# Performance work log

Measured on AMD Instinct MI355X. Metric: run time of the kernel, lower is better.

The kernel has to match this reference:

```python
import jax, jax.numpy as jnp
import numpy as np

B, L, PD, DIM, H, DH, DEPTH, MLP, NIMG, NCLS, TH = 2, 2048, 768, 512, 8, 64, 2, 2048, 4, 1000, 32


def _ln(x, g):
    # bias-free LayerNorm (beta buffer is zeros), eps matches torch F.layer_norm
    mu = jnp.mean(x, axis=-1, keepdims=True)
    var = jnp.var(x, axis=-1, keepdims=True)
    return (x - mu) / jnp.sqrt(var + 1e-5) * g


def _rms(x, g):
    # F.normalize(dim=-1) * sqrt(dim_head) * gamma; x: [b,h,n,dh], g: [h,1,dh]
    n = jnp.linalg.norm(x, axis=-1, keepdims=True)
    return x / jnp.maximum(n, 1e-12) * (DH ** 0.5) * g


def _attn(x, context, mask, ln_g, qg, kg, Wq, Wkv, Wo):
    b, n = x.shape[0], x.shape[1]
    xn = _ln(x, ln_g)
    kv = xn if context is None else context  # context is NOT pre-normed (matches source)
    m = kv.shape[1]
    q = (xn @ Wq).reshape(b, n, H, DH).transpose(0, 2, 1, 3)   # [b,h,n,dh]
    k, v = jnp.split(kv @ Wkv, 2, axis=-1)
    k = k.reshape(b, m, H, DH).transpose(0, 2, 1, 3)
    v = v.reshape(b, m, H, DH).transpose(0, 2, 1, 3)
    q = _rms(q, qg)
    k = _rms(k, kg)
    dots = jnp.einsum('bhid,bhjd->bhij', q, k)  # no 1/sqrt(d): QK-RMSNorm carries the scale
    neg = -jnp.finfo(dots.dtype).max
    dots = jnp.where(mask, dots, neg)
    a = jax.nn.softmax(dots, axis=-1)
    out = jnp.einsum('bhij,bhjd->bhid', a, v)
    out = out.transpose(0, 2, 1, 3).reshape(b, n, H * DH)
    return out @ Wo


def _forward(patches, ln_pe1_g, W_pe, b_pe, ln_pe2_g, pos_h_emb, pos_w_emb,
             attn_ln_g, q_g, k_g, Wq, Wkv, Wo, ff_ln_g, W1, b1, W2, b2,
             final_ln_g, pool_q, pool_ln_g, pool_q_g, pool_k_g,
             pool_Wq, pool_Wkv, pool_Wo, head_ln_g, W_head,
             pos_h, pos_w, image_ids):
    # patch embedding: LN -> Linear -> LN, then factorized 2D pos embed
    x = _ln(patches, ln_pe1_g) @ W_pe + b_pe
    x = _ln(x, ln_pe2_g)
    x = x + pos_h_emb[pos_h] + pos_w_emb[pos_w]
    # block-diagonal attention mask: tokens attend only within their image
    mask = (image_ids[:, None, :, None] == image_ids[:, None, None, :])  # [B,1,L,L]
    for i in range(DEPTH):
        x = _attn(x, None, mask, attn_ln_g[i], q_g[i], k_g[i], Wq[i], Wkv[i], Wo[i]) + x
        h = _ln(x, ff_ln_g[i]) @ W1[i] + b1[i]
        h = jax.nn.gelu(h, approximate=False)
        x = h @ W2[i] + b2[i] + x
    x = _ln(x, final_ln_g)
    # attention pooling: one learned query per packed image
    queries = jnp.broadcast_to(pool_q, (B, NIMG, DIM))
    pmask = (jnp.arange(NIMG)[None, None, :, None] == image_ids[:, None, None, :])  # [B,1,NIMG,L]
    pooled = _attn(queries, x, pmask, pool_ln_g, pool_q_g, pool_k_g, pool_Wq, pool_Wkv, pool_Wo) + queries
    return _ln(pooled, head_ln_g) @ W_head  # [B, NIMG, NCLS]


def setup_inputs() -> dict:
    key = jax.random.key(0)
    ks = jax.random.split(key, 16)
    s = 0.02
    inp = {}
    inp['patches'] = jax.random.normal(ks[0], (B, L, PD), jnp.float32)
    inp['pos_h'] = jax.random.randint(ks[1], (B, L), 0, TH)
    inp['pos_w'] = jax.random.randint(ks[2], (B, L), 0, TH)
    inp['image_ids'] = jnp.sort(jax.random.randint(ks[3], (B, L), 0, NIMG), axis=-1)
    inp['ln_pe1_g'] = jnp.ones((PD,), jnp.float32)
    inp['W_pe'] = jax.random.normal(ks[4], (PD, DIM), jnp.float32) * s
    inp['b_pe'] = jnp.zeros((DIM,), jnp.float32)
    inp['ln_pe2_g'] = jnp.ones((DIM,), jnp.float32)
    inp['pos_h_emb'] = jax.random.normal(ks[5], (TH, DIM), jnp.float32)
    inp['pos_w_emb'] = jax.random.normal(ks[6], (TH, DIM), jnp.float32)
    inp['attn_ln_g'] = jnp.ones((DEPTH, DIM), jnp.float32)
    inp['q_g'] = jnp.ones((DEPTH, H, 1, DH), jnp.float32)
    inp['k_g'] = jnp.ones((DEPTH, H, 1, DH), jnp.float32)
    inp['Wq'] = jax.random.normal(ks[7], (DEPTH, DIM, H * DH), jnp.float32) * s
    inp['Wkv'] = jax.random.normal(ks[8], (DEPTH, DIM, 2 * H * DH), jnp.float32) * s
    inp['Wo'] = jax.random.normal(ks[9], (DEPTH, H * DH, DIM), jnp.float32) * s
    inp['ff_ln_g'] = jnp.ones((DEPTH, DIM), jnp.float32)
    inp['W1'] = jax.random.normal(ks[10], (DEPTH, DIM, MLP), jnp.float32) * s
    inp['b1'] = jnp.zeros((DEPTH, MLP), jnp.float32)
    inp['W2'] = jax.random.normal(ks[11], (DEPTH, MLP, DIM), jnp.float32) * s
    inp['b2'] = jnp.zeros((DEPTH, DIM), jnp.float32)
    inp['final_ln_g'] = jnp.ones((DIM,), jnp.float32)
    inp['pool_q'] = jax.random.normal(ks[12], (DIM,), jnp.float32)
    inp['pool_ln_g'] = jnp.ones((DIM,), jnp.float32)
    inp['pool_q_g'] = jnp.ones((H, 1, DH), jnp.float32)
    inp['pool_k_g'] = jnp.ones((H, 1, DH), jnp.float32)
    inp['pool_Wq'] = jax.random.normal(ks[13], (DIM, H * DH), jnp.float32) * s
    inp['pool_Wkv'] = jax.random.normal(ks[14], (DIM, 2 * H * DH), jnp.float32) * s
    inp['pool_Wo'] = jax.random.normal(ks[15], (H * DH, DIM), jnp.float32) * s
    inp['head_ln_g'] = jnp.ones((DIM,), jnp.float32)
    inp['W_head'] = jax.random.normal(jax.random.fold_in(key, 99), (DIM, NCLS), jnp.float32) * s
    return inp


def reference(patches, pos_h, pos_w, image_ids, ln_pe1_g, W_pe, b_pe, ln_pe2_g,
              pos_h_emb, pos_w_emb, attn_ln_g, q_g, k_g, Wq, Wkv, Wo, ff_ln_g,
              W1, b1, W2, b2, final_ln_g, pool_q, pool_ln_g, pool_q_g, pool_k_g,
              pool_Wq, pool_Wkv, pool_Wo, head_ln_g, W_head):
    return _forward(patches, ln_pe1_g, W_pe, b_pe, ln_pe2_g, pos_h_emb, pos_w_emb,
                    attn_ln_g, q_g, k_g, Wq, Wkv, Wo, ff_ln_g, W1, b1, W2, b2,
                    final_ln_g, pool_q, pool_ln_g, pool_q_g, pool_k_g,
                    pool_Wq, pool_Wkv, pool_Wo, head_ln_g, W_head,
                    pos_h, pos_w, image_ids)
```

## Files before the change

kernel.cpp:

```cpp
#include <hip/hip_runtime.h>
#include <hip/hip_bf16.h>
#include <cfloat>
#include <math.h>

#define BB 2
#define LL 2048
#define PD 768
#define DIM 512
#define HH 8
#define DH 64
#define DEPTH 2
#define MLP 2048
#define NIMG 4
#define NCLS 1000
#define ROWS (BB*LL)
#define QKV (3*DIM)
#define NEGBIG (-1e30f)

typedef __hip_bfloat16 bf16;
typedef __bf16 v8bf __attribute__((ext_vector_type(8)));
typedef float f32x4 __attribute__((ext_vector_type(4)));

__device__ __forceinline__ float ldin(const void* p, size_t i, int bf) {
    return bf ? __bfloat162float(((const bf16*)p)[i]) : ((const float*)p)[i];
}
__device__ __forceinline__ float lda(const float* p, size_t i) { return p[i]; }
__device__ __forceinline__ float lda(const bf16* p, size_t i) { return __bfloat162float(p[i]); }
__device__ __forceinline__ void st(float* p, size_t i, float v) { p[i] = v; }
__device__ __forceinline__ void st(bf16* p, size_t i, float v) { p[i] = __float2bfloat16(v); }
__device__ __forceinline__ unsigned short f2bf(float x) {
    return __builtin_bit_cast(unsigned short, __float2bfloat16(x));
}
__device__ __forceinline__ float us2f(unsigned short u) {
    return __bfloat162float(__builtin_bit_cast(bf16, u));
}

__device__ __forceinline__ void stage16(const void* gsrc, void* ldst)
{
    __builtin_amdgcn_global_load_lds(
        (const __attribute__((address_space(1))) unsigned int*)(unsigned long long)gsrc,
        (__attribute__((address_space(3))) unsigned int*)(unsigned int)(unsigned long long)ldst,
        16, 0, 0);
}

__global__ void detect_dtype_kernel(const void* ones, int* flag)
{
    if (threadIdx.x == 0 && blockIdx.x == 0)
        *flag = (((const unsigned*)ones)[0] == 0x3F803F80u) ? 1 : 0;
}

__global__ void wconv_kernel(const void* __restrict__ W, int K, int N, size_t inStride,
                             bf16* __restrict__ out, size_t outOff, size_t outStride,
                             const int* dtf)
{
    __shared__ float t[32][33];
    const int bf = *dtf;
    const size_t zin = (size_t)blockIdx.z * inStride;
    const size_t zout = outOff + (size_t)blockIdx.z * outStride;
    const int kb = blockIdx.y * 32, nb = blockIdx.x * 32;
    const int tx = threadIdx.x, ty = threadIdx.y;
    #pragma unroll
    for (int u = 0; u < 4; ++u)
        t[ty + 8 * u][tx] = ldin(W, zin + (size_t)(kb + ty + 8 * u) * N + nb + tx, bf);
    __syncthreads();
    #pragma unroll
    for (int u = 0; u < 4; ++u)
        out[zout + (size_t)(nb + ty + 8 * u) * K + kb + tx] = __float2bfloat16(t[tx][ty + 8 * u]);
}

template<int RAWIN, typename TOUT>
__global__ void ln_kernel(const void* __restrict__ in, const void* __restrict__ g, size_t goff,
                          TOUT* __restrict__ out, int D, const int* dtf)
{
    __shared__ float red[16];
    const int bf = *dtf;
    const int row = blockIdx.x, tid = threadIdx.x;
    const size_t base = (size_t)row * D;
    float s = 0.f, ss = 0.f;
    for (int d = tid; d < D; d += blockDim.x) {
        float v = RAWIN ? ldin(in, base + d, bf) : ((const float*)in)[base + d];
        s += v; ss += v * v;
    }
    for (int o = 32; o; o >>= 1) { s += __shfl_xor(s, o); ss += __shfl_xor(ss, o); }
    const int wid = tid >> 6, lane = tid & 63, nw = blockDim.x >> 6;
    if (lane == 0) { red[wid] = s; red[8 + wid] = ss; }
    __syncthreads();
    if (tid == 0) {
        float a = 0.f, b = 0.f;
        for (int w = 0; w < nw; ++w) { a += red[w]; b += red[8 + w]; }
        red[0] = a; red[8] = b;
    }
    __syncthreads();
    const float mean = red[0] / D;
    const float var  = red[8] / D - mean * mean;
    const float rstd = rsqrtf(var + 1e-5f);
    for (int d = tid; d < D; d += blockDim.x) {
        float v = RAWIN ? ldin(in, base + d, bf) : ((const float*)in)[base + d];
        st(out, base + d, (v - mean) * rstd * ldin(g, goff + d, bf));
    }
}

__global__ void patch_fuse_kernel(const float* __restrict__ part,
                                  const void* __restrict__ b_pe,
                                  const void* __restrict__ g1,
                                  const void* __restrict__ phe, const void* __restrict__ pwe,
                                  const int* __restrict__ ph, const int* __restrict__ pw,
                                  const void* __restrict__ g2,
                                  float* __restrict__ x, bf16* __restrict__ xb,
                                  const int* dtf)
{
    __shared__ float red[16];
    const int bf = *dtf;
    const int row = blockIdx.x, tid = threadIdx.x;
    const size_t base = (size_t)row * DIM;
    const int wid = tid >> 6, lane = tid & 63;
    float v[2];
    float s = 0.f, ss = 0.f;
    #pragma unroll
    for (int u = 0; u < 2; ++u) {
        const int d = tid + 256 * u;
        float a = part[base + d] + part[(size_t)ROWS * DIM + base + d] + ldin(b_pe, d, bf);
        v[u] = a; s += a; ss += a * a;
    }
    for (int o = 32; o; o >>= 1) { s += __shfl_xor(s, o); ss += __shfl_xor(ss, o); }
    if (lane == 0) { red[wid] = s; red[8 + wid] = ss; }
    __syncthreads();
    if (tid == 0) {
        float a = 0.f, b = 0.f;
        for (int w2 = 0; w2 < 4; ++w2) { a += red[w2]; b += red[8 + w2]; }
        red[0] = a; red[8] = b;
    }
    __syncthreads();
    {
        const float mean = red[0] / DIM;
        const float var  = red[8] / DIM - mean * mean;
        const float rstd = rsqrtf(var + 1e-5f);
        const size_t hoff = (size_t)ph[row] * DIM, woff = (size_t)pw[row] * DIM;
        s = 0.f; ss = 0.f;
        #pragma unroll
        for (int u = 0; u < 2; ++u) {
            const int d = tid + 256 * u;
            float a = (v[u] - mean) * rstd * ldin(g1, d, bf)
                    + ldin(phe, hoff + d, bf) + ldin(pwe, woff + d, bf);
            x[base + d] = a;
            v[u] = a; s += a; ss += a * a;
        }
    }
    for (int o = 32; o; o >>= 1) { s += __shfl_xor(s, o); ss += __shfl_xor(ss, o); }
    __syncthreads();
    if (lane == 0) { red[wid] = s; red[8 + wid] = ss; }
    __syncthreads();
    if (tid == 0) {
        float a = 0.f, b = 0.f;
        for (int w2 = 0; w2 < 4; ++w2) { a += red[w2]; b += red[8 + w2]; }
        red[0] = a; red[8] = b;
    }
    __syncthreads();
    const float mean = red[0] / DIM;
    const float var  = red[8] / DIM - mean * mean;
    const float rstd = rsqrtf(var + 1e-5f);
    #pragma unroll
    for (int u = 0; u < 2; ++u) {
        const int d = tid + 256 * u;
        xb[base + d] = __float2bfloat16((v[u] - mean) * rstd * ldin(g2, d, bf));
    }
}

#define GM 128
#define GN 64
#define GK 64

template<typename TO, int EPI>
__global__ void mgemm_kernel(const bf16* __restrict__ A, const bf16* __restrict__ Wt,
                             const void* __restrict__ bias, size_t boff,
                             const float* __restrict__ resid, TO* __restrict__ out,
                             int M, int N, int K, int kc, int gelu, const int* dtf)
{
    __shared__ __align__(16) unsigned short As[2][GM][GK];
    __shared__ __align__(16) unsigned short Bs[2][GN][GK];
    const int tid = threadIdx.x;
    const int w = tid >> 6, l = tid & 63, g = l >> 4, c = l & 15;
    const int wm = (w >> 1) * 64, wn = (w & 1) * 32;
    const int m0 = blockIdx.y * GM, n0 = blockIdx.x * GN;
    const int kbeg = blockIdx.z * kc;
    const int lrow = l >> 3, lcol = (l & 7) * 8;

#define STAGE_MG(BUF, K0)                                                          \
    {                                                                              \
        _Pragma("unroll")                                                          \
        for (int u = 0; u < 4; ++u) {                                              \
            const int rr = 32 * w + 8 * u;                                         \
            stage16(A + (size_t)(m0 + rr + lrow) * K + (K0) + lcol, &As[BUF][rr][0]); \
        }                                                                          \
        _Pragma("unroll")                                                          \
        for (int u = 0; u < 2; ++u) {                                              \
            const int rr = 16 * w + 8 * u;                                         \
            stage16(Wt + (size_t)(n0 + rr + lrow) * K + (K0) + lcol, &Bs[BUF][rr][0]); \
        }                                                                          \
    }

    f32x4 acc[4][2] = {};
    const int nt = kc / GK;
    STAGE_MG(0, kbeg);
    int cur = 0;
    for (int t = 0; t < nt; ++t) {
        if (t + 1 < nt) {
            STAGE_MG(cur ^ 1, kbeg + (t + 1) * GK);
            asm volatile("s_waitcnt vmcnt(6)" ::: "memory");
        } else {
            asm volatile("s_waitcnt vmcnt(0)" ::: "memory");
        }
        __builtin_amdgcn_s_barrier();
        __builtin_amdgcn_sched_barrier(0);
        #pragma unroll
        for (int kk = 0; kk < GK; kk += 32) {
            v8bf av[4], bv[2];
            #pragma unroll
            for (int i = 0; i < 4; ++i) av[i] = *(const v8bf*)&As[cur][wm + i * 16 + c][kk + 8 * g];
            #pragma unroll
            for (int j = 0; j < 2; ++j) bv[j] = *(const v8bf*)&Bs[cur][wn + j * 16 + c][kk + 8 * g];
            #pragma unroll
            for (int i = 0; i < 4; ++i)
                #pragma unroll
                for (int j = 0; j < 2; ++j)
                    acc[i][j] = __builtin_amdgcn_mfma_f32_16x16x32_bf16(av[i], bv[j], acc[i][j], 0, 0, 0);
        }
        __builtin_amdgcn_s_barrier();
        cur ^= 1;
    }
#undef STAGE_MG

    if (EPI == 0) {
        float* po = (float*)out + (size_t)blockIdx.z * M * N;
        #pragma unroll
        for (int i = 0; i < 4; ++i) {
            const int rb = m0 + wm + i * 16 + 4 * g;
            #pragma unroll
            for (int j = 0; j < 2; ++j) {
                const int col = n0 + wn + j * 16 + c;
                #pragma unroll
                for (int r = 0; r < 4; ++r)
                    po[(size_t)(rb + r) * N + col] = acc[i][j][r];
            }
        }
    } else {
        const int bf = *dtf;
        #pragma unroll
        for (int i = 0; i < 4; ++i) {
            const int rb = m0 + wm + i * 16 + 4 * g;
            #pragma unroll
            for (int j = 0; j < 2; ++j) {
                const int col = n0 + wn + j * 16 + c;
                const float bvl = bias ? ldin(bias, boff + col, bf) : 0.f;
                #pragma unroll
                for (int r = 0; r < 4; ++r) {
                    float v = acc[i][j][r] + bvl;
                    if (gelu) v = 0.5f * v * (1.f + erff(v * 0.70710678118654752f));
                    if (resid) v += resid[(size_t)(rb + r) * N + col];
                    st(out, (size_t)(rb + r) * N + col, v);
                }
            }
        }
    }
}

__global__ void comb_ln_kernel(const float* __restrict__ part, int S,
                               const void* __restrict__ bias, size_t boff,
                               float* __restrict__ x, const void* __restrict__ g, size_t goff,
                               bf16* __restrict__ xb, const int* dtf)
{
    __shared__ float red[16];
    const int bf = *dtf;
    const int row = blockIdx.x, tid = threadIdx.x;
    const size_t base = (size_t)row * DIM;
    float v[2];
    float s = 0.f, ss = 0.f;
    #pragma unroll
    for (int u = 0; u < 2; ++u) {
        const int d = tid + 256 * u;
        float a = 0.f;
        for (int sc = 0; sc < S; ++sc) a += part[(size_t)sc * ROWS * DIM + base + d];
        if (bias) a += ldin(bias, boff + d, bf);
        a += x[base + d];
        x[base + d] = a;
        v[u] = a; s += a; ss += a * a;
    }
    for (int o = 32; o; o >>= 1) { s += __shfl_xor(s, o); ss += __shfl_xor(ss, o); }
    const int wid = tid >> 6, lane = tid & 63;
    if (lane == 0) { red[wid] = s; red[8 + wid] = ss; }
    __syncthreads();
    if (tid == 0) {
        float a = 0.f, b = 0.f;
        for (int w2 = 0; w2 < 4; ++w2) { a += red[w2]; b += red[8 + w2]; }
        red[0] = a; red[8] = b;
    }
    __syncthreads();
    const float mean = red[0] / DIM;
    const float var  = red[8] / DIM - mean * mean;
    const float rstd = rsqrtf(var + 1e-5f);
    #pragma unroll
    for (int u = 0; u < 2; ++u) {
        const int d = tid + 256 * u;
        xb[base + d] = __float2bfloat16((v[u] - mean) * rstd * ldin(g, goff + d, bf));
    }
}

#define TS 16
template<typename TA, typename TO>
__global__ void gemm_kernel(const TA* __restrict__ A, const void* __restrict__ W, size_t woff,
                            const void* __restrict__ bias, size_t boff,
                            const float* __restrict__ resid, TO* __restrict__ out,
                            int M, int N, int K, int gelu, const int* dtf)
{
    __shared__ float As[TS][TS + 1];
    __shared__ float Bs[TS][TS + 1];
    const int bf = *dtf;
    const int tx = threadIdx.x, ty = threadIdx.y;
    const int col = blockIdx.x * TS + tx;
    const int row = blockIdx.y * TS + ty;
    float acc = 0.f;
    for (int k0 = 0; k0 < K; k0 += TS) {
        const int ka = k0 + tx;
        As[ty][tx] = (row < M && ka < K) ? lda(A, (size_t)row * K + ka) : 0.f;
        const int kb = k0 + ty;
        Bs[ty][tx] = (col < N && kb < K) ? ldin(W, woff + (size_t)kb * N + col, bf) : 0.f;
        __syncthreads();
        #pragma unroll
        for (int kk = 0; kk < TS; ++kk) acc = fmaf(As[ty][kk], Bs[kk][tx], acc);
        __syncthreads();
    }
    if (row < M && col < N) {
        if (bias) acc += ldin(bias, boff + col, bf);
        if (gelu) acc = 0.5f * acc * (1.f + erff(acc * 0.70710678118654752f));
        if (resid) acc += resid[(size_t)row * N + col];
        st(out, (size_t)row * N + col, acc);
    }
}

__global__ void rms_kernel(float* __restrict__ buf, const void* __restrict__ g, size_t goff,
                           int stride, int colbase, const int* dtf)
{
    const int bf = *dtf;
    const int r = blockIdx.x, h = blockIdx.y, lane = threadIdx.x;
    float* p = buf + (size_t)r * stride + colbase + h * DH;
    const float v = p[lane];
    float ss = v * v;
    for (int o = 32; o; o >>= 1) ss += __shfl_xor(ss, o);
    const float norm = sqrtf(ss);
    const float sc = 8.0f / fmaxf(norm, 1e-12f);
    p[lane] = v * sc * ldin(g, goff + h * DH + lane, bf);
}

__global__ void rms2_kernel(bf16* __restrict__ buf, int stride,
                            const void* __restrict__ g0, size_t g0off,
                            int base1, const void* __restrict__ g1, size_t g1off,
                            int nslot, const int* dtf)
{
    const int bf = *dtf;
    const int tid = threadIdx.x;
    const int s = tid >> 4, li = tid & 15;
    if (s >= nslot) return;
    const int h = s & 7;
    const int colbase = (s < 8) ? 0 : base1;
    const void* g = (s < 8) ? g0 : g1;
    const size_t go = ((s < 8) ? g0off : g1off) + h * DH + li * 4;
    bf16* p = buf + (size_t)blockIdx.x * stride + colbase + h * DH + li * 4;
    ushort4 v = *(const ushort4*)p;
    const float f0 = us2f(v.x), f1 = us2f(v.y), f2 = us2f(v.z), f3 = us2f(v.w);
    float ss = f0 * f0 + f1 * f1 + f2 * f2 + f3 * f3;
    ss += __shfl_xor(ss, 8); ss += __shfl_xor(ss, 4);
    ss += __shfl_xor(ss, 2); ss += __shfl_xor(ss, 1);
    const float sc = 8.0f / fmaxf(sqrtf(ss), 1e-12f);
    ushort4 o;
    o.x = f2bf(f0 * sc * ldin(g, go + 0, bf));
    o.y = f2bf(f1 * sc * ldin(g, go + 1, bf));
    o.z = f2bf(f2 * sc * ldin(g, go + 2, bf));
    o.w = f2bf(f3 * sc * ldin(g, go + 3, bf));
    *(ushort4*)p = o;
}

#define QT 64
#define KT 64
#define LP 72

__global__ void flash_attn_kernel(const bf16* __restrict__ q, int qstr,
                                  const bf16* __restrict__ kpt, const bf16* __restrict__ vpt,
                                  int kvstr, const int* __restrict__ ids,
                                  const void* __restrict__ qg, const void* __restrict__ kg,
                                  size_t goff, bf16* __restrict__ out, const int* dtf)
{
    __shared__ __align__(16) unsigned short Qs[QT][LP];
    __shared__ __align__(16) unsigned short Ks[KT][LP];
    __shared__ __align__(16) unsigned short Vt[DH][LP];
    __shared__ __align__(16) unsigned short Ps[QT][LP];
    __shared__ __align__(16) int ids_s[KT];
    __shared__ __align__(16) int qids_s[QT];
    __shared__ int range_s[2];

    const int bf = *dtf;
    const int tid = threadIdx.x;
    const int bid = blockIdx.x;
    const int s0 = (bid & 7) * 64 + (bid >> 3);
    const int qb = (s0 & 31) * QT;
    const int h = (s0 >> 5) & 7;
    const int b = s0 >> 8;
    const int w = tid >> 6, l = tid & 63, g = l >> 4, c = l & 15;

    const int r4 = tid >> 2, c16 = (tid & 3) << 4;

    float gk[16];
    #pragma unroll
    for (int j = 0; j < 16; ++j) gk[j] = ldin(kg, goff + h * DH + c16 + j, bf);

    {
        const bf16* qp = q + (size_t)(b * LL + qb + r4) * qstr + h * DH + c16;
        int4 raw0 = *(const int4*)qp;
        int4 raw1 = *(const int4*)(qp + 8);
        const unsigned short* u0 = (const unsigned short*)&raw0;
        const unsigned short* u1 = (const unsigned short*)&raw1;
        float f[16];
        float ssq = 0.f;
        #pragma unroll
        for (int j = 0; j < 8; ++j) { f[j] = us2f(u0[j]); f[8 + j] = us2f(u1[j]); }
        #pragma unroll
        for (int j = 0; j < 16; ++j) ssq += f[j] * f[j];
        ssq += __shfl_xor(ssq, 1); ssq += __shfl_xor(ssq, 2);
        const float sc = 8.0f / fmaxf(sqrtf(ssq), 1e-12f);
        ushort4 pk[4];
        unsigned short* pp = (unsigned short*)pk;
        #pragma unroll
        for (int j = 0; j < 16; ++j)
            pp[j] = f2bf(f[j] * sc * ldin(qg, goff + h * DH + c16 + j, bf));
        *(ushort4*)&Qs[r4][c16]      = pk[0];
        *(ushort4*)&Qs[r4][c16 + 4]  = pk[1];
        *(ushort4*)&Qs[r4][c16 + 8]  = pk[2];
        *(ushort4*)&Qs[r4][c16 + 12] = pk[3];
        if (tid < QT) qids_s[tid] = ids[b * LL + qb + tid];
    }
    if (tid == 0) {
        const int* bp = ids + b * LL;
        const int qlo = bp[qb], qhi = bp[qb + QT - 1];
        int lo = 0, hi = LL;
        while (lo < hi) { int mid = (lo + hi) >> 1; if (bp[mid] < qlo) lo = mid + 1; else hi = mid; }
        range_s[0] = lo;
        int lo2 = 0, hi2 = LL;
        while (lo2 < hi2) { int mid = (lo2 + hi2) >> 1; if (bp[mid] <= qhi) lo2 = mid + 1; else hi2 = mid; }
        range_s[1] = lo2;
    }
    __syncthreads();

    const int myid = qids_s[16 * w + c];
    const v8bf qf0 = *(const v8bf*)&Qs[16 * w + c][8 * g];
    const v8bf qf1 = *(const v8bf*)&Qs[16 * w + c][8 * g + 32];
    const int kb_start = (range_s[0] / KT) * KT;
    const int kb_end = range_s[1];

    f32x4 o[4];
    #pragma unroll
    for (int dt = 0; dt < 4; ++dt) o[dt] = (f32x4){0.f, 0.f, 0.f, 0.f};
    float mr = NEGBIG, lr = 0.f;

    for (int kb = kb_start; kb < kb_end; kb += KT) {
        __syncthreads();
        {
            const bf16* kp = kpt + (size_t)(b * LL + kb + r4) * kvstr + h * DH + c16;
            int4 raw0 = *(const int4*)kp;
            int4 raw1 = *(const int4*)(kp + 8);
            const unsigned short* u0 = (const unsigned short*)&raw0;
            const unsigned short* u1 = (const unsigned short*)&raw1;
            float f[16];
            float ssq = 0.f;
            #pragma unroll
            for (int j = 0; j < 8; ++j) { f[j] = us2f(u0[j]); f[8 + j] = us2f(u1[j]); }
            #pragma unroll
            for (int j = 0; j < 16; ++j) ssq += f[j] * f[j];
            ssq += __shfl_xor(ssq, 1); ssq += __shfl_xor(ssq, 2);
            const float sc = 8.0f / fmaxf(sqrtf(ssq), 1e-12f);
            ushort4 pk[4];
            unsigned short* pp = (unsigned short*)pk;
            #pragma unroll
            for (int j = 0; j < 16; ++j) pp[j] = f2bf(f[j] * sc * gk[j]);
            *(ushort4*)&Ks[r4][c16]      = pk[0];
            *(ushort4*)&Ks[r4][c16 + 4]  = pk[1];
            *(ushort4*)&Ks[r4][c16 + 8]  = pk[2];
            *(ushort4*)&Ks[r4][c16 + 12] = pk[3];
        }
        {
            const int kp2 = (tid & 31) * 2, db = (tid >> 5) * 8;
            const bf16* v0p = vpt + (size_t)(b * LL + kb + kp2) * kvstr + h * DH + db;
            const bf16* v1p = v0p + kvstr;
            const ushort4 a0 = *(const ushort4*)v0p;
            const ushort4 a1 = *(const ushort4*)(v0p + 4);
            const ushort4 b0 = *(const ushort4*)v1p;
            const ushort4 b1 = *(const ushort4*)(v1p + 4);
            const unsigned short* ap0 = (const unsigned short*)&a0;
            const unsigned short* ap1 = (const unsigned short*)&a1;
            const unsigned short* bp0 = (const unsigned short*)&b0;
            const unsigned short* bp1 = (const unsigned short*)&b1;
            #pragma unroll
            for (int j = 0; j < 4; ++j) {
                *(unsigned int*)&Vt[db + j][kp2]     = (unsigned)ap0[j] | ((unsigned)bp0[j] << 16);
                *(unsigned int*)&Vt[db + 4 + j][kp2] = (unsigned)ap1[j] | ((unsigned)bp1[j] << 16);
            }
        }
        if (tid < KT) ids_s[tid] = ids[b * LL + kb + tid];
        __syncthreads();

        f32x4 stt[4];
        __builtin_amdgcn_s_setprio(1);
        #pragma unroll
        for (int t = 0; t < 4; ++t) {
            stt[t] = (f32x4){0.f, 0.f, 0.f, 0.f};
            v8bf kf0 = *(const v8bf*)&Ks[16 * t + c][8 * g];
            v8bf kf1 = *(const v8bf*)&Ks[16 * t + c][8 * g + 32];
            stt[t] = __builtin_amdgcn_mfma_f32_16x16x32_bf16(kf0, qf0, stt[t], 0, 0, 0);
            stt[t] = __builtin_amdgcn_mfma_f32_16x16x32_bf16(kf1, qf1, stt[t], 0, 0, 0);
        }
        __builtin_amdgcn_s_setprio(0);

        float sv[16]; int mk[16];
        float tmax = NEGBIG;
        #pragma unroll
        for (int t = 0; t < 4; ++t) {
            int4 iv = *(const int4*)&ids_s[16 * t + 4 * g];
            const int* ivp = (const int*)&iv;
            #pragma unroll
            for (int r = 0; r < 4; ++r) {
                float s = stt[t][r];
                int m = (ivp[r] == myid);
                sv[4 * t + r] = s; mk[4 * t + r] = m;
                if (m) tmax = fmaxf(tmax, s);
            }
        }
        tmax = fmaxf(tmax, __shfl_xor(tmax, 16));
        tmax = fmaxf(tmax, __shfl_xor(tmax, 32));
        const float mnew = fmaxf(mr, tmax);
        const float al = __expf(mr - mnew);
        float tsum = 0.f;
        #pragma unroll
        for (int t = 0; t < 4; ++t) {
            ushort4 pk;
            unsigned short* pp = (unsigned short*)&pk;
            #pragma unroll
            for (int r = 0; r < 4; ++r) {
                float p = mk[4 * t + r] ? __expf(sv[4 * t + r] - mnew) : 0.f;
                tsum += p;
                pp[r] = f2bf(p);
            }
            *(ushort4*)&Ps[16 * w + c][16 * t + 4 * g] = pk;
        }
        tsum += __shfl_xor(tsum, 16);
        tsum += __shfl_xor(tsum, 32);
        lr = lr * al + tsum;
        mr = mnew;

        const float a0 = __shfl(al, 4 * g + 0);
        const float a1 = __shfl(al, 4 * g + 1);
        const float a2 = __shfl(al, 4 * g + 2);
        const float a3 = __shfl(al, 4 * g + 3);
        #pragma unroll
        for (int dt = 0; dt < 4; ++dt) {
            o[dt][0] *= a0; o[dt][1] *= a1; o[dt][2] *= a2; o[dt][3] *= a3;
        }

        const v8bf pf0 = *(const v8bf*)&Ps[16 * w + c][8 * g];
        const v8bf pf1 = *(const v8bf*)&Ps[16 * w + c][8 * g + 32];
        __builtin_amdgcn_s_setprio(1);
        #pragma unroll
        for (int dt = 0; dt < 4; ++dt) {
            v8bf vf0 = *(const v8bf*)&Vt[16 * dt + c][8 * g];
            v8bf vf1 = *(const v8bf*)&Vt[16 * dt + c][8 * g + 32];
            o[dt] = __builtin_amdgcn_mfma_f32_16x16x32_bf16(pf0, vf0, o[dt], 0, 0, 0);
            o[dt] = __builtin_amdgcn_mfma_f32_16x16x32_bf16(pf1, vf1, o[dt], 0, 0, 0);
        }
        __builtin_amdgcn_s_setprio(0);
    }

    const float li0 = 1.f / __shfl(lr, 4 * g + 0);
    const float li1 = 1.f / __shfl(lr, 4 * g + 1);
    const float li2 = 1.f / __shfl(lr, 4 * g + 2);
    const float li3 = 1.f / __shfl(lr, 4 * g + 3);
    #pragma unroll
    for (int dt = 0; dt < 4; ++dt) {
        bf16* op = out + (size_t)(b * LL + qb + 16 * w) * DIM + h * DH + 16 * dt + c;
        op[(size_t)(4 * g + 0) * DIM] = __float2bfloat16(o[dt][0] * li0);
        op[(size_t)(4 * g + 1) * DIM] = __float2bfloat16(o[dt][1] * li1);
        op[(size_t)(4 * g + 2) * DIM] = __float2bfloat16(o[dt][2] * li2);
        op[(size_t)(4 * g + 3) * DIM] = __float2bfloat16(o[dt][3] * li3);
    }
}

#define PCH 16
#define PCK (LL / PCH)

__global__ void pool_attn_part_kernel(const float* __restrict__ q, const bf16* __restrict__ kv,
                                      int kvs, const int* __restrict__ ids,
                                      float* __restrict__ ppm, float* __restrict__ ppl,
                                      float* __restrict__ ppo)
{
    const int iq = blockIdx.x & (NIMG - 1), ch = blockIdx.x >> 2;
    const int h = blockIdx.y, b = blockIdx.z;
    const int tid = threadIdx.x;
    const int qrow = b * NIMG + iq;
    const int j0 = ch * PCK;
    __shared__ float qs[DH];
    __shared__ float s[PCK];

    qs[tid] = q[(size_t)qrow * DIM + h * DH + tid];
    __syncthreads();
    #pragma unroll
    for (int u = 0; u < 2; ++u) {
        const int j = j0 + tid + 64 * u;
        const bf16* kp = kv + (size_t)(b * LL + j) * kvs + h * DH;
        float d = 0.f;
        #pragma unroll
        for (int t = 0; t < DH; t += 8) {
            int4 kvv = *(const int4*)&kp[t];
            const unsigned short* uu = (const unsigned short*)&kvv;
            #pragma unroll
            for (int z = 0; z < 8; ++z) d = fmaf(qs[t + z], us2f(uu[z]), d);
        }
        s[tid + 64 * u] = (ids[b * LL + j] == iq) ? d : NEGBIG;
    }
    __syncthreads();
    float m = fmaxf(s[tid], s[tid + 64]);
    for (int o = 32; o; o >>= 1) m = fmaxf(m, __shfl_xor(m, o));
    const float p0 = __expf(s[tid] - m), p1 = __expf(s[tid + 64] - m);
    float ls = p0 + p1;
    for (int o = 32; o; o >>= 1) ls += __shfl_xor(ls, o);
    s[tid] = p0; s[tid + 64] = p1;
    __syncthreads();
    float acc = 0.f;
    for (int jj = 0; jj < PCK; ++jj)
        acc += s[jj] * __bfloat162float(kv[(size_t)(b * LL + j0 + jj) * kvs + DIM + h * DH + tid]);
    const int p = ((b * HH + h) * NIMG + iq) * PCH + ch;
    if (tid == 0) { ppm[p] = m; ppl[p] = ls; }
    ppo[(size_t)p * DH + tid] = acc;
}

__global__ void pool_attn_comb_kernel(const float* __restrict__ ppm, const float* __restrict__ ppl,
                                      const float* __restrict__ ppo, float* __restrict__ out)
{
    const int iq = blockIdx.x, h = blockIdx.y, b = blockIdx.z;
    const int d = threadIdx.x;
    const int pb = ((b * HH + h) * NIMG + iq) * PCH;
    float mstar = NEGBIG;
    #pragma unroll
    for (int ch = 0; ch < PCH; ++ch) mstar = fmaxf(mstar, ppm[pb + ch]);
    float lsum = 0.f, osum = 0.f;
    #pragma unroll
    for (int ch = 0; ch < PCH; ++ch) {
        const float w = __expf(ppm[pb + ch] - mstar);
        lsum += ppl[pb + ch] * w;
        osum += ppo[(size_t)(pb + ch) * DH + d] * w;
    }
    out[(size_t)(b * NIMG + iq) * DIM + h * DH + d] = osum / lsum;
}

__global__ void fill_q_kernel(float* __restrict__ queries, const void* __restrict__ pool_q,
                              const int* dtf)
{
    const int bf = *dtf;
    const int idx = blockIdx.x * blockDim.x + threadIdx.x;
    if (idx < BB * NIMG * DIM) queries[idx] = ldin(pool_q, idx % DIM, bf);
}

__global__ void write_out_kernel(const float* __restrict__ in, void* __restrict__ out, int n,
                                 const int* dtf)
{
    const int bf = *dtf;
    const int idx = blockIdx.x * blockDim.x + threadIdx.x;
    if (idx < n) {
        if (bf) ((bf16*)out)[idx] = __float2bfloat16(in[idx]);
        else    ((float*)out)[idx] = in[idx];
    }
}

extern "C" void kernel_launch(void* const* d_in, const int* in_sizes, int n_in,
                              void* d_out, int out_size, void* d_ws, size_t ws_size,
                              hipStream_t stream)
{
    const void* patches   = d_in[0];
    const int*  pos_h     = (const int*) d_in[1];
    const int*  pos_w     = (const int*) d_in[2];
    const int*  image_ids = (const int*) d_in[3];
    const void* ln_pe1_g  = d_in[4];
    const void* W_pe      = d_in[5];
    const void* b_pe      = d_in[6];
    const void* ln_pe2_g  = d_in[7];
    const void* pos_h_emb = d_in[8];
    const void* pos_w_emb = d_in[9];
    const void* attn_ln_g = d_in[10];
    const void* q_g       = d_in[11];
    const void* k_g       = d_in[12];
    const void* Wq        = d_in[13];
    const void* Wkv       = d_in[14];
    const void* Wo        = d_in[15];
    const void* ff_ln_g   = d_in[16];
    const void* W1        = d_in[17];
    const void* b1        = d_in[18];
    const void* W2        = d_in[19];
    const void* b2        = d_in[20];
    const void* final_ln_g= d_in[21];
    const void* pool_q    = d_in[22];
    const void* pool_ln_g = d_in[23];
    const void* pool_q_g  = d_in[24];
    const void* pool_k_g  = d_in[25];
    const void* pool_Wq   = d_in[26];
    const void* pool_Wkv  = d_in[27];
    const void* pool_Wo   = d_in[28];
    const void* head_ln_g = d_in[29];
    const void* W_head    = d_in[30];

    char* p = (char*)d_ws;
    int* flag = (int*)p;                         p += 256;
    float* x   = (float*)p;                      p += (size_t)ROWS * DIM * 4;
    bf16* xb   = (bf16*)p;                       p += (size_t)ROWS * PD * 2;
    bf16* qkvb = (bf16*)p;  bf16* hb = qkvb;     p += (size_t)ROWS * MLP * 2;
    bf16* wpeT  = (bf16*)p;                      p += (size_t)DIM * PD * 2;
    bf16* wqkvT = (bf16*)p;                      p += (size_t)DEPTH * QKV * DIM * 2;
    bf16* woT   = (bf16*)p;                      p += (size_t)DEPTH * DIM * DIM * 2;
    bf16* w1T   = (bf16*)p;                      p += (size_t)DEPTH * MLP * DIM * 2;
    bf16* w2T   = (bf16*)p;                      p += (size_t)DEPTH * DIM * MLP * 2;
    bf16* pkvT  = (bf16*)p;                      p += (size_t)2 * DIM * DIM * 2;
    float* queries = (float*)p;                  p += 4096 * 4;
    float* qp      = (float*)p;                  p += 4096 * 4;
    float* pattn   = (float*)p;                  p += 4096 * 4;
    float* pooled  = (float*)p;                  p += 4096 * 4;
    bf16*  pln     = (bf16*)p;                   p += 4096 * 2;
    float* hout    = (float*)p;                  p += 8192 * 4;
    float* ppm     = (float*)p;                  p += 1024 * 4;
    float* ppl     = (float*)p;                  p += 1024 * 4;
    float* ppo     = (float*)p;                  p += (size_t)1024 * DH * 4;
    float* part    = (float*)p;                  p += (size_t)4 * ROWS * DIM * 4;

    const dim3 blk256(256);
    const dim3 blkG(TS, TS);
    const dim3 blkT(32, 8);

    detect_dtype_kernel<<<1, 1, 0, stream>>>(ln_pe1_g, flag);

    wconv_kernel<<<dim3(DIM / 32, PD / 32, 1), blkT, 0, stream>>>(
        W_pe, PD, DIM, 0, wpeT, 0, 0, flag);
    wconv_kernel<<<dim3(DIM / 32, DIM / 32, DEPTH), blkT, 0, stream>>>(
        Wq, DIM, DIM, (size_t)DIM * DIM, wqkvT, 0, (size_t)QKV * DIM, flag);
    wconv_kernel<<<dim3(2 * DIM / 32, DIM / 32, DEPTH), blkT, 0, stream>>>(
        Wkv, DIM, 2 * DIM, (size_t)DIM * 2 * DIM, wqkvT, (size_t)DIM * DIM, (size_t)QKV * DIM, flag);
    wconv_kernel<<<dim3(DIM / 32, DIM / 32, DEPTH), blkT, 0, stream>>>(
        Wo, DIM, DIM, (size_t)DIM * DIM, woT, 0, (size_t)DIM * DIM, flag);
    wconv_kernel<<<dim3(MLP / 32, DIM / 32, DEPTH), blkT, 0, stream>>>(
        W1, DIM, MLP, (size_t)DIM * MLP, w1T, 0, (size_t)MLP * DIM, flag);
    wconv_kernel<<<dim3(DIM / 32, MLP / 32, DEPTH), blkT, 0, stream>>>(
        W2, MLP, DIM, (size_t)MLP * DIM, w2T, 0, (size_t)DIM * MLP, flag);
    wconv_kernel<<<dim3(2 * DIM / 32, DIM / 32, 1), blkT, 0, stream>>>(
        pool_Wkv, DIM, 2 * DIM, 0, pkvT, 0, 0, flag);

    ln_kernel<1, bf16><<<ROWS, blk256, 0, stream>>>(patches, ln_pe1_g, 0, xb, PD, flag);
    mgemm_kernel<float, 0><<<dim3(DIM / GN, ROWS / GM, 2), blk256, 0, stream>>>(
        xb, wpeT, nullptr, 0, nullptr, part, ROWS, DIM, PD, PD / 2, 0, flag);
    patch_fuse_kernel<<<ROWS, blk256, 0, stream>>>(
        part, b_pe, ln_pe2_g, pos_h_emb, pos_w_emb, pos_h, pos_w, attn_ln_g, x, xb, flag);

    for (int i = 0; i < DEPTH; ++i) {
        mgemm_kernel<bf16, 1><<<dim3(QKV / GN, ROWS / GM, 1), blk256, 0, stream>>>(
            xb, wqkvT + (size_t)i * QKV * DIM, nullptr, 0, nullptr, qkvb,
            ROWS, QKV, DIM, DIM, 0, flag);
        flash_attn_kernel<<<dim3(512), blk256, 0, stream>>>(
            qkvb, QKV, qkvb + DIM, qkvb + 2 * DIM, QKV, image_ids,
            q_g, k_g, (size_t)i * HH * DH, xb, flag);
        mgemm_kernel<float, 0><<<dim3(DIM / GN, ROWS / GM, 2), blk256, 0, stream>>>(
            xb, woT + (size_t)i * DIM * DIM, nullptr, 0, nullptr, part,
            ROWS, DIM, DIM, DIM / 2, 0, flag);
        comb_ln_kernel<<<ROWS, blk256, 0, stream>>>(
            part, 2, nullptr, 0, x, ff_ln_g, (size_t)i * DIM, xb, flag);
        mgemm_kernel<bf16, 1><<<dim3(MLP / GN, ROWS / GM, 1), blk256, 0, stream>>>(
            xb, w1T + (size_t)i * MLP * DIM, b1, (size_t)i * MLP, nullptr, hb,
            ROWS, MLP, DIM, DIM, 1, flag);
        mgemm_kernel<float, 0><<<dim3(DIM / GN, ROWS / GM, 4), blk256, 0, stream>>>(
            hb, w2T + (size_t)i * DIM * MLP, nullptr, 0, nullptr, part,
            ROWS, DIM, MLP, MLP / 4, 0, flag);
        const void* gnext = (i + 1 < DEPTH) ? attn_ln_g : final_ln_g;
        const size_t gnoff = (i + 1 < DEPTH) ? (size_t)(i + 1) * DIM : 0;
        comb_ln_kernel<<<ROWS, blk256, 0, stream>>>(
            part, 4, b2, (size_t)i * DIM, x, gnext, gnoff, xb, flag);
    }

    fill_q_kernel<<<(BB * NIMG * DIM + 255) / 256, blk256, 0, stream>>>(queries, pool_q, flag);
    ln_kernel<0, bf16><<<BB * NIMG, blk256, 0, stream>>>(queries, pool_ln_g, 0, pln, DIM, flag);
    gemm_kernel<bf16, float><<<dim3(DIM / TS, 1), blkG, 0, stream>>>(
        pln, pool_Wq, 0, nullptr, 0, nullptr, qp, BB * NIMG, DIM, DIM, 0, flag);
    mgemm_kernel<bf16, 1><<<dim3(2 * DIM / GN, ROWS / GM, 1), blk256, 0, stream>>>(
        xb, pkvT, nullptr, 0, nullptr, qkvb, ROWS, 2 * DIM, DIM, DIM, 0, flag);
    rms_kernel<<<dim3(BB * NIMG, HH), dim3(64), 0, stream>>>(
        qp, pool_q_g, 0, DIM, 0, flag);
    rms2_kernel<<<ROWS, blk256, 0, stream>>>(
        qkvb, 2 * DIM, pool_k_g, 0, 0, nullptr, 0, 8, flag);
    pool_attn_part_kernel<<<dim3(NIMG * PCH, HH, BB), dim3(64), 0, stream>>>(
        qp, qkvb, 2 * DIM, image_ids, ppm, ppl, ppo);
    pool_attn_comb_kernel<<<dim3(NIMG, HH, BB), dim3(64), 0, stream>>>(ppm, ppl, ppo, pattn);
    gemm_kernel<float, float><<<dim3(DIM / TS, 1), blkG, 0, stream>>>(
        pattn, pool_Wo, 0, nullptr, 0, queries, pooled, BB * NIMG, DIM, DIM, 0, flag);

    ln_kernel<0, bf16><<<BB * NIMG, blk256, 0, stream>>>(pooled, head_ln_g, 0, pln, DIM, flag);
    gemm_kernel<bf16, float><<<dim3((NCLS + TS - 1) / TS, 1), blkG, 0, stream>>>(
        pln, W_head, 0, nullptr, 0, nullptr, hout, BB * NIMG, NCLS, DIM, 0, flag);
    write_out_kernel<<<(BB * NIMG * NCLS + 255) / 256, blk256, 0, stream>>>(
        hout, d_out, BB * NIMG * NCLS, flag);
}
```

Baseline: 463.8 us.

## Split flash attention over two KV halves and fuse pooling head tail kernels

```diff
diff --git a/kernel.cpp b/kernel.cpp
--- a/kernel.cpp
+++ b/kernel.cpp
@@ -16,6 +16,8 @@
 #define ROWS (BB*LL)
 #define QKV (3*DIM)
 #define NEGBIG (-1e30f)
+#define BHL (BB*HH*LL)
+#define BHLD ((size_t)BHL*DH)
 
 typedef __hip_bfloat16 bf16;
 typedef __bf16 v8bf __attribute__((ext_vector_type(8)));
@@ -24,8 +26,6 @@
 __device__ __forceinline__ float ldin(const void* p, size_t i, int bf) {
     return bf ? __bfloat162float(((const bf16*)p)[i]) : ((const float*)p)[i];
 }
-__device__ __forceinline__ float lda(const float* p, size_t i) { return p[i]; }
-__device__ __forceinline__ float lda(const bf16* p, size_t i) { return __bfloat162float(p[i]); }
 __device__ __forceinline__ void st(float* p, size_t i, float v) { p[i] = v; }
 __device__ __forceinline__ void st(bf16* p, size_t i, float v) { p[i] = __float2bfloat16(v); }
 __device__ __forceinline__ unsigned short f2bf(float x) {
@@ -68,9 +68,8 @@
         out[zout + (size_t)(nb + ty + 8 * u) * K + kb + tx] = __float2bfloat16(t[tx][ty + 8 * u]);
 }
 
-template<int RAWIN, typename TOUT>
-__global__ void ln_kernel(const void* __restrict__ in, const void* __restrict__ g, size_t goff,
-                          TOUT* __restrict__ out, int D, const int* dtf)
+__global__ void ln_raw_kernel(const void* __restrict__ in, const void* __restrict__ g,
+                              bf16* __restrict__ out, int D, const int* dtf)
 {
     __shared__ float red[16];
     const int bf = *dtf;
@@ -78,7 +77,7 @@
     const size_t base = (size_t)row * D;
     float s = 0.f, ss = 0.f;
     for (int d = tid; d < D; d += blockDim.x) {
-        float v = RAWIN ? ldin(in, base + d, bf) : ((const float*)in)[base + d];
+        float v = ldin(in, base + d, bf);
         s += v; ss += v * v;
     }
     for (int o = 32; o; o >>= 1) { s += __shfl_xor(s, o); ss += __shfl_xor(ss, o); }
@@ -95,8 +94,8 @@
     const float var  = red[8] / D - mean * mean;
     const float rstd = rsqrtf(var + 1e-5f);
     for (int d = tid; d < D; d += blockDim.x) {
-        float v = RAWIN ? ldin(in, base + d, bf) : ((const float*)in)[base + d];
-        st(out, base + d, (v - mean) * rstd * ldin(g, goff + d, bf));
+        float v = ldin(in, base + d, bf);
+        out[base + d] = __float2bfloat16((v - mean) * rstd * ldin(g, d, bf));
     }
 }
 
@@ -305,66 +304,16 @@
     }
 }
 
-#define TS 16
-template<typename TA, typename TO>
-__global__ void gemm_kernel(const TA* __restrict__ A, const void* __restrict__ W, size_t woff,
-                            const void* __restrict__ bias, size_t boff,
-                            const float* __restrict__ resid, TO* __restrict__ out,
-                            int M, int N, int K, int gelu, const int* dtf)
-{
-    __shared__ float As[TS][TS + 1];
-    __shared__ float Bs[TS][TS + 1];
-    const int bf = *dtf;
-    const int tx = threadIdx.x, ty = threadIdx.y;
-    const int col = blockIdx.x * TS + tx;
-    const int row = blockIdx.y * TS + ty;
-    float acc = 0.f;
-    for (int k0 = 0; k0 < K; k0 += TS) {
-        const int ka = k0 + tx;
-        As[ty][tx] = (row < M && ka < K) ? lda(A, (size_t)row * K + ka) : 0.f;
-        const int kb = k0 + ty;
-        Bs[ty][tx] = (col < N && kb < K) ? ldin(W, woff + (size_t)kb * N + col, bf) : 0.f;
-        __syncthreads();
-        #pragma unroll
-        for (int kk = 0; kk < TS; ++kk) acc = fmaf(As[ty][kk], Bs[kk][tx], acc);
-        __syncthreads();
-    }
-    if (row < M && col < N) {
-        if (bias) acc += ldin(bias, boff + col, bf);
-        if (gelu) acc = 0.5f * acc * (1.f + erff(acc * 0.70710678118654752f));
-        if (resid) acc += resid[(size_t)row * N + col];
-        st(out, (size_t)row * N + col, acc);
-    }
-}
-
-__global__ void rms_kernel(float* __restrict__ buf, const void* __restrict__ g, size_t goff,
-                           int stride, int colbase, const int* dtf)
-{
-    const int bf = *dtf;
-    const int r = blockIdx.x, h = blockIdx.y, lane = threadIdx.x;
-    float* p = buf + (size_t)r * stride + colbase + h * DH;
-    const float v = p[lane];
-    float ss = v * v;
-    for (int o = 32; o; o >>= 1) ss += __shfl_xor(ss, o);
-    const float norm = sqrtf(ss);
-    const float sc = 8.0f / fmaxf(norm, 1e-12f);
-    p[lane] = v * sc * ldin(g, goff + h * DH + lane, bf);
-}
-
 __global__ void rms2_kernel(bf16* __restrict__ buf, int stride,
-                            const void* __restrict__ g0, size_t g0off,
-                            int base1, const void* __restrict__ g1, size_t g1off,
-                            int nslot, const int* dtf)
+                            const void* __restrict__ g0, size_t g0off, int nslot, const int* dtf)
 {
     const int bf = *dtf;
     const int tid = threadIdx.x;
     const int s = tid >> 4, li = tid & 15;
     if (s >= nslot) return;
     const int h = s & 7;
-    const int colbase = (s < 8) ? 0 : base1;
-    const void* g = (s < 8) ? g0 : g1;
-    const size_t go = ((s < 8) ? g0off : g1off) + h * DH + li * 4;
-    bf16* p = buf + (size_t)blockIdx.x * stride + colbase + h * DH + li * 4;
+    const size_t go = g0off + h * DH + li * 4;
+    bf16* p = buf + (size_t)blockIdx.x * stride + h * DH + li * 4;
     ushort4 v = *(const ushort4*)p;
     const float f0 = us2f(v.x), f1 = us2f(v.y), f2 = us2f(v.z), f3 = us2f(v.w);
     float ss = f0 * f0 + f1 * f1 + f2 * f2 + f3 * f3;
@@ -372,10 +321,10 @@
     ss += __shfl_xor(ss, 2); ss += __shfl_xor(ss, 1);
     const float sc = 8.0f / fmaxf(sqrtf(ss), 1e-12f);
     ushort4 o;
-    o.x = f2bf(f0 * sc * ldin(g, go + 0, bf));
-    o.y = f2bf(f1 * sc * ldin(g, go + 1, bf));
-    o.z = f2bf(f2 * sc * ldin(g, go + 2, bf));
-    o.w = f2bf(f3 * sc * ldin(g, go + 3, bf));
+    o.x = f2bf(f0 * sc * ldin(g0, go + 0, bf));
+    o.y = f2bf(f1 * sc * ldin(g0, go + 1, bf));
+    o.z = f2bf(f2 * sc * ldin(g0, go + 2, bf));
+    o.w = f2bf(f3 * sc * ldin(g0, go + 3, bf));
     *(ushort4*)p = o;
 }
 
@@ -383,11 +332,12 @@
 #define KT 64
 #define LP 72
 
-__global__ void flash_attn_kernel(const bf16* __restrict__ q, int qstr,
+__global__ void flash_part_kernel(const bf16* __restrict__ q, int qstr,
                                   const bf16* __restrict__ kpt, const bf16* __restrict__ vpt,
                                   int kvstr, const int* __restrict__ ids,
                                   const void* __restrict__ qg, const void* __restrict__ kg,
-                                  size_t goff, bf16* __restrict__ out, const int* dtf)
+                                  size_t goff, float* __restrict__ pm, float* __restrict__ pl,
+                                  float* __restrict__ po, const int* dtf)
 {
     __shared__ __align__(16) unsigned short Qs[QT][LP];
     __shared__ __align__(16) unsigned short Ks[KT][LP];
@@ -400,10 +350,11 @@
     const int bf = *dtf;
     const int tid = threadIdx.x;
     const int bid = blockIdx.x;
-    const int s0 = (bid & 7) * 64 + (bid >> 3);
-    const int qb = (s0 & 31) * QT;
-    const int h = (s0 >> 5) & 7;
-    const int b = s0 >> 8;
+    const int s0 = (bid & 7) * 128 + (bid >> 3);
+    const int half = s0 & 1;
+    const int qb = ((s0 >> 1) & 31) * QT;
+    const int h = (s0 >> 6) & 7;
+    const int b = s0 >> 9;
     const int w = tid >> 6, l = tid & 63, g = l >> 4, c = l & 15;
 
     const int r4 = tid >> 2, c16 = (tid & 3) << 4;
@@ -452,8 +403,12 @@
     const int myid = qids_s[16 * w + c];
     const v8bf qf0 = *(const v8bf*)&Qs[16 * w + c][8 * g];
     const v8bf qf1 = *(const v8bf*)&Qs[16 * w + c][8 * g + 32];
-    const int kb_start = (range_s[0] / KT) * KT;
-    const int kb_end = range_s[1];
+    const int ts = (range_s[0] / KT) * KT;
+    const int te = range_s[1];
+    const int ntile = (te - ts + KT - 1) / KT;
+    const int h0 = (ntile + 1) >> 1;
+    const int kb_start = ts + (half ? h0 * KT : 0);
+    const int kb_end = half ? te : ((ts + h0 * KT) < te ? (ts + h0 * KT) : te);
 
     f32x4 o[4];
     #pragma unroll
@@ -576,18 +531,35 @@
         __builtin_amdgcn_s_setprio(0);
     }
 
-    const float li0 = 1.f / __shfl(lr, 4 * g + 0);
-    const float li1 = 1.f / __shfl(lr, 4 * g + 1);
-    const float li2 = 1.f / __shfl(lr, 4 * g + 2);
-    const float li3 = 1.f / __shfl(lr, 4 * g + 3);
+    const size_t qbase = (size_t)(b * HH + h) * LL + qb;
+    if (g == 0) {
+        pm[(size_t)half * BHL + qbase + 16 * w + c] = mr;
+        pl[(size_t)half * BHL + qbase + 16 * w + c] = lr;
+    }
     #pragma unroll
     for (int dt = 0; dt < 4; ++dt) {
-        bf16* op = out + (size_t)(b * LL + qb + 16 * w) * DIM + h * DH + 16 * dt + c;
-        op[(size_t)(4 * g + 0) * DIM] = __float2bfloat16(o[dt][0] * li0);
-        op[(size_t)(4 * g + 1) * DIM] = __float2bfloat16(o[dt][1] * li1);
-        op[(size_t)(4 * g + 2) * DIM] = __float2bfloat16(o[dt][2] * li2);
-        op[(size_t)(4 * g + 3) * DIM] = __float2bfloat16(o[dt][3] * li3);
-    }
+        float* op = po + (size_t)half * BHLD + (qbase + 16 * w) * DH + 16 * dt + c;
+        op[(size_t)(4 * g + 0) * DH] = o[dt][0];
+        op[(size_t)(4 * g + 1) * DH] = o[dt][1];
+        op[(size_t)(4 * g + 2) * DH] = o[dt][2];
+        op[(size_t)(4 * g + 3) * DH] = o[dt][3];
+    }
+}
+
+__global__ void flash_comb_kernel(const float* __restrict__ pm, const float* __restrict__ pl,
+                                  const float* __restrict__ po, bf16* __restrict__ out)
+{
+    const int h = blockIdx.y, b = blockIdx.z;
+    const int qrow = blockIdx.x * 4 + (threadIdx.x >> 6);
+    const int d = threadIdx.x & 63;
+    const size_t qg = (size_t)(b * HH + h) * LL + qrow;
+    const float m0 = pm[qg], m1 = pm[BHL + qg];
+    const float l0 = pl[qg], l1 = pl[BHL + qg];
+    const float ms = fmaxf(m0, m1);
+    const float w0 = __expf(m0 - ms), w1 = __expf(m1 - ms);
+    const float num = w0 * po[qg * DH + d] + w1 * po[BHLD + qg * DH + d];
+    const float den = w0 * l0 + w1 * l1;
+    out[((size_t)b * LL + qrow) * DIM + h * DH + d] = __float2bfloat16(num / den);
 }
 
 #define PCH 16
@@ -601,12 +573,11 @@
     const int iq = blockIdx.x & (NIMG - 1), ch = blockIdx.x >> 2;
     const int h = blockIdx.y, b = blockIdx.z;
     const int tid = threadIdx.x;
-    const int qrow = b * NIMG + iq;
     const int j0 = ch * PCK;
     __shared__ float qs[DH];
     __shared__ float s[PCK];
 
-    qs[tid] = q[(size_t)qrow * DIM + h * DH + tid];
+    qs[tid] = q[h * DH + tid];
     __syncthreads();
     #pragma unroll
     for (int u = 0; u < 2; ++u) {
@@ -657,22 +628,100 @@
     out[(size_t)(b * NIMG + iq) * DIM + h * DH + d] = osum / lsum;
 }
 
-__global__ void fill_q_kernel(float* __restrict__ queries, const void* __restrict__ pool_q,
-                              const int* dtf)
-{
+__global__ void pool_q_fuse_kernel(const void* __restrict__ pool_q, const void* __restrict__ pln_g,
+                                   const void* __restrict__ Wq, const void* __restrict__ qg,
+                                   float* __restrict__ qp, const int* dtf)
+{
+    __shared__ float xs[DIM];
+    __shared__ float os[DIM];
+    __shared__ float red[16];
     const int bf = *dtf;
-    const int idx = blockIdx.x * blockDim.x + threadIdx.x;
-    if (idx < BB * NIMG * DIM) queries[idx] = ldin(pool_q, idx % DIM, bf);
-}
-
-__global__ void write_out_kernel(const float* __restrict__ in, void* __restrict__ out, int n,
+    const int tid = threadIdx.x;
+    const int w = tid >> 6, l = tid & 63;
+    float v0 = ldin(pool_q, tid, bf), v1 = ldin(pool_q, tid + 256, bf);
+    float s = v0 + v1, ss = v0 * v0 + v1 * v1;
+    for (int o = 32; o; o >>= 1) { s += __shfl_xor(s, o); ss += __shfl_xor(ss, o); }
+    if (l == 0) { red[w] = s; red[8 + w] = ss; }
+    __syncthreads();
+    if (tid == 0) {
+        float a = 0.f, b = 0.f;
+        for (int w2 = 0; w2 < 4; ++w2) { a += red[w2]; b += red[8 + w2]; }
+        red[0] = a; red[8] = b;
+    }
+    __syncthreads();
+    const float mean = red[0] / DIM;
+    const float var  = red[8] / DIM - mean * mean;
+    const float rstd = rsqrtf(var + 1e-5f);
+    xs[tid]       = (v0 - mean) * rstd * ldin(pln_g, tid, bf);
+    xs[tid + 256] = (v1 - mean) * rstd * ldin(pln_g, tid + 256, bf);
+    __syncthreads();
+    float a0 = 0.f, a1 = 0.f;
+    for (int k = 0; k < DIM; ++k) {
+        const float xv = xs[k];
+        a0 = fmaf(xv, ldin(Wq, (size_t)k * DIM + tid, bf), a0);
+        a1 = fmaf(xv, ldin(Wq, (size_t)k * DIM + tid + 256, bf), a1);
+    }
+    os[tid] = a0; os[tid + 256] = a1;
+    __syncthreads();
+    const float e1 = os[w * 64 + l], e2 = os[256 + w * 64 + l];
+    float s1 = e1 * e1, s2 = e2 * e2;
+    for (int o = 32; o; o >>= 1) { s1 += __shfl_xor(s1, o); s2 += __shfl_xor(s2, o); }
+    qp[w * 64 + l]       = e1 * (8.0f / fmaxf(sqrtf(s1), 1e-12f)) * ldin(qg, w * 64 + l, bf);
+    qp[256 + w * 64 + l] = e2 * (8.0f / fmaxf(sqrtf(s2), 1e-12f)) * ldin(qg, 256 + w * 64 + l, bf);
+}
+
+__global__ void head_fuse_kernel(const float* __restrict__ pattn, const void* __restrict__ Wo,
+                                 const void* __restrict__ pool_q, const void* __restrict__ hg,
+                                 const void* __restrict__ Wh, void* __restrict__ out,
                                  const int* dtf)
 {
+    __shared__ float xs[DIM];
+    __shared__ float ps[DIM];
+    __shared__ float red[16];
     const int bf = *dtf;
-    const int idx = blockIdx.x * blockDim.x + threadIdx.x;
-    if (idx < n) {
-        if (bf) ((bf16*)out)[idx] = __float2bfloat16(in[idx]);
-        else    ((float*)out)[idx] = in[idx];
+    const int row = blockIdx.x, tid = threadIdx.x;
+    const int w = tid >> 6, l = tid & 63;
+    xs[tid] = pattn[(size_t)row * DIM + tid];
+    xs[tid + 256] = pattn[(size_t)row * DIM + tid + 256];
+    __syncthreads();
+    float a0 = ldin(pool_q, tid, bf), a1 = ldin(pool_q, tid + 256, bf);
+    for (int k = 0; k < DIM; ++k) {
+        const float xv = xs[k];
+        a0 = fmaf(xv, ldin(Wo, (size_t)k * DIM + tid, bf), a0);
+        a1 = fmaf(xv, ldin(Wo, (size_t)k * DIM + tid + 256, bf), a1);
+    }
+    float s = a0 + a1, ss = a0 * a0 + a1 * a1;
+    for (int o = 32; o; o >>= 1) { s += __shfl_xor(s, o); ss += __shfl_xor(ss, o); }
+    if (l == 0) { red[w] = s; red[8 + w] = ss; }
+    __syncthreads();
+    if (tid == 0) {
+        float a = 0.f, b = 0.f;
+        for (int w2 = 0; w2 < 4; ++w2) { a += red[w2]; b += red[8 + w2]; }
+        red[0] = a; red[8] = b;
+    }
+    __syncthreads();
+    const float mean = red[0] / DIM;
+    const float var  = red[8] / DIM - mean * mean;
+    const float rstd = rsqrtf(var + 1e-5f);
+    ps[tid]       = (a0 - mean) * rstd * ldin(hg, tid, bf);
+    ps[tid + 256] = (a1 - mean) * rstd * ldin(hg, tid + 256, bf);
+    __syncthreads();
+    float hacc[4] = {0.f, 0.f, 0.f, 0.f};
+    for (int k = 0; k < DIM; ++k) {
+        const float xv = ps[k];
+        #pragma unroll
+        for (int u = 0; u < 4; ++u) {
+            const int col = tid + 256 * u;
+            if (col < NCLS) hacc[u] = fmaf(xv, ldin(Wh, (size_t)k * NCLS + col, bf), hacc[u]);
+        }
+    }
+    #pragma unroll
+    for (int u = 0; u < 4; ++u) {
+        const int col = tid + 256 * u;
+        if (col < NCLS) {
+            if (bf) ((bf16*)out)[(size_t)row * NCLS + col] = __float2bfloat16(hacc[u]);
+            else    ((float*)out)[(size_t)row * NCLS + col] = hacc[u];
+        }
     }
 }
 
@@ -723,19 +772,17 @@
     bf16* w1T   = (bf16*)p;                      p += (size_t)DEPTH * MLP * DIM * 2;
     bf16* w2T   = (bf16*)p;                      p += (size_t)DEPTH * DIM * MLP * 2;
     bf16* pkvT  = (bf16*)p;                      p += (size_t)2 * DIM * DIM * 2;
-    float* queries = (float*)p;                  p += 4096 * 4;
     float* qp      = (float*)p;                  p += 4096 * 4;
     float* pattn   = (float*)p;                  p += 4096 * 4;
-    float* pooled  = (float*)p;                  p += 4096 * 4;
-    bf16*  pln     = (bf16*)p;                   p += 4096 * 2;
-    float* hout    = (float*)p;                  p += 8192 * 4;
     float* ppm     = (float*)p;                  p += 1024 * 4;
     float* ppl     = (float*)p;                  p += 1024 * 4;
     float* ppo     = (float*)p;                  p += (size_t)1024 * DH * 4;
+    float* pm      = (float*)p;                  p += (size_t)2 * BHL * 4;
+    float* pl      = (float*)p;                  p += (size_t)2 * BHL * 4;
     float* part    = (float*)p;                  p += (size_t)4 * ROWS * DIM * 4;
+    float* po      = part;
 
     const dim3 blk256(256);
-    const dim3 blkG(TS, TS);
     const dim3 blkT(32, 8);
 
     detect_dtype_kernel<<<1, 1, 0, stream>>>(ln_pe1_g, flag);
@@ -755,7 +802,7 @@
     wconv_kernel<<<dim3(2 * DIM / 32, DIM / 32, 1), blkT, 0, stream>>>(
         pool_Wkv, DIM, 2 * DIM, 0, pkvT, 0, 0, flag);
 
-    ln_kernel<1, bf16><<<ROWS, blk256, 0, stream>>>(patches, ln_pe1_g, 0, xb, PD, flag);
+    ln_raw_kernel<<<ROWS, blk256, 0, stream>>>(patches, ln_pe1_g, xb, PD, flag);
     mgemm_kernel<float, 0><<<dim3(DIM / GN, ROWS / GM, 2), blk256, 0, stream>>>(
         xb, wpeT, nullptr, 0, nullptr, part, ROWS, DIM, PD, PD / 2, 0, flag);
     patch_fuse_kernel<<<ROWS, blk256, 0, stream>>>(
@@ -765,9 +812,10 @@
         mgemm_kernel<bf16, 1><<<dim3(QKV / GN, ROWS / GM, 1), blk256, 0, stream>>>(
             xb, wqkvT + (size_t)i * QKV * DIM, nullptr, 0, nullptr, qkvb,
             ROWS, QKV, DIM, DIM, 0, flag);
-        flash_attn_kernel<<<dim3(512), blk256, 0, stream>>>(
+        flash_part_kernel<<<dim3(1024), blk256, 0, stream>>>(
             qkvb, QKV, qkvb + DIM, qkvb + 2 * DIM, QKV, image_ids,
-            q_g, k_g, (size_t)i * HH * DH, xb, flag);
+            q_g, k_g, (size_t)i * HH * DH, pm, pl, po, flag);
+        flash_comb_kernel<<<dim3(LL / 4, HH, BB), blk256, 0, stream>>>(pm, pl, po, xb);
         mgemm_kernel<float, 0><<<dim3(DIM / GN, ROWS / GM, 2), blk256, 0, stream>>>(
             xb, woT + (size_t)i * DIM * DIM, nullptr, 0, nullptr, part,
             ROWS, DIM, DIM, DIM / 2, 0, flag);
@@ -785,25 +833,13 @@
             part, 4, b2, (size_t)i * DIM, x, gnext, gnoff, xb, flag);
     }
 
-    fill_q_kernel<<<(BB * NIMG * DIM + 255) / 256, blk256, 0, stream>>>(queries, pool_q, flag);
-    ln_kernel<0, bf16><<<BB * NIMG, blk256, 0, stream>>>(queries, pool_ln_g, 0, pln, DIM, flag);
-    gemm_kernel<bf16, float><<<dim3(DIM / TS, 1), blkG, 0, stream>>>(
-        pln, pool_Wq, 0, nullptr, 0, nullptr, qp, BB * NIMG, DIM, DIM, 0, flag);
+    pool_q_fuse_kernel<<<1, blk256, 0, stream>>>(pool_q, pool_ln_g, pool_Wq, pool_q_g, qp, flag);
     mgemm_kernel<bf16, 1><<<dim3(2 * DIM / GN, ROWS / GM, 1), blk256, 0, stream>>>(
         xb, pkvT, nullptr, 0, nullptr, qkvb, ROWS, 2 * DIM, DIM, DIM, 0, flag);
-    rms_kernel<<<dim3(BB * NIMG, HH), dim3(64), 0, stream>>>(
-        qp, pool_q_g, 0, DIM, 0, flag);
-    rms2_kernel<<<ROWS, blk256, 0, stream>>>(
-        qkvb, 2 * DIM, pool_k_g, 0, 0, nullptr, 0, 8, flag);
+    rms2_kernel<<<ROWS, blk256, 0, stream>>>(qkvb, 2 * DIM, pool_k_g, 0, 8, flag);
     pool_attn_part_kernel<<<dim3(NIMG * PCH, HH, BB), dim3(64), 0, stream>>>(
         qp, qkvb, 2 * DIM, image_ids, ppm, ppl, ppo);
     pool_attn_comb_kernel<<<dim3(NIMG, HH, BB), dim3(64), 0, stream>>>(ppm, ppl, ppo, pattn);
-    gemm_kernel<float, float><<<dim3(DIM / TS, 1), blkG, 0, stream>>>(
-        pattn, pool_Wo, 0, nullptr, 0, queries, pooled, BB * NIMG, DIM, DIM, 0, flag);
-
-    ln_kernel<0, bf16><<<BB * NIMG, blk256, 0, stream>>>(pooled, head_ln_g, 0, pln, DIM, flag);
-    gemm_kernel<bf16, float><<<dim3((NCLS + TS - 1) / TS, 1), blkG, 0, stream>>>(
-        pln, W_head, 0, nullptr, 0, nullptr, hout, BB * NIMG, NCLS, DIM, 0, flag);
-    write_out_kernel<<<(BB * NIMG * NCLS + 255) / 256, blk256, 0, stream>>>(
-        hout, d_out, BB * NIMG * NCLS, flag);
-}
+    head_fuse_kernel<<<dim3(BB * NIMG), blk256, 0, stream>>>(
+        pattn, pool_Wo, pool_q, head_ln_g, W_head, d_out, flag);
+}
```

New measurement: 1.088 ms. +134.6%, slower.
